# Optimization experiments

Hardware: AMD Instinct MI355X
Metric: run time of the kernel (lower is better)

## Reference

```python
import jax, jax.numpy as jnp
import numpy as np

NUM_HEADS = 4
K_RATIO = 0.01
K_NEIGHBORS = 8
DIM = 256


def setup_inputs() -> dict:
    key = jax.random.key(0)
    ks = jax.random.split(key, 11)
    d, nh = DIM, NUM_HEADS
    def lin(k, out_f, in_f):
        return jax.random.normal(k, (out_f, in_f), jnp.float32) / np.sqrt(in_f)
    return {
        "x": jax.random.normal(ks[0], (32, d, 64, 64), jnp.float32),
        # graph_modulator: Conv2d(d, d//4, 1) -> ReLU -> Conv2d(d//4, nh, 1) -> Sigmoid
        "gm_w1": lin(ks[1], d // 4, d),
        "gm_b1": jnp.zeros((d // 4,), jnp.float32),
        "gm_w2": lin(ks[2], nh, d // 4),
        "gm_b2": jnp.zeros((nh,), jnp.float32),
        # local_qkv: Linear(d, 3d, bias=False)
        "qkv_w": lin(ks[3], 3 * d, d),
        # graph_encoder: Linear(d, d//2) -> ReLU -> Linear(d//2, nh)
        "ge_w1": lin(ks[4], d // 2, d),
        "ge_b1": jnp.zeros((d // 2,), jnp.float32),
        "ge_w2": lin(ks[5], nh, d // 2),
        "ge_b2": jnp.zeros((nh,), jnp.float32),
    }


def _forward(x, gm_w1, gm_b1, gm_w2, gm_b2, qkv_w, ge_w1, ge_b1, ge_w2, ge_b2):
    B, C, H, W = x.shape
    nh = NUM_HEADS
    hd = C // nh
    scale = hd ** -0.5
    HW = H * W

    # spatial modulation: two 1x1 convs
    h1 = jax.nn.relu(jnp.einsum("bchw,oc->bohw", x, gm_w1) + gm_b1[None, :, None, None])
    spatial_mod = jax.nn.sigmoid(jnp.einsum("bchw,oc->bohw", h1, gm_w2) + gm_b2[None, :, None, None])  # [B,nh,H,W]

    # top-k pixel selection by mean-abs importance
    num_select = min(max(1, int(HW * K_RATIO)), 64)  # static
    importance = jnp.mean(jnp.abs(x), axis=1).reshape(B, HW)
    _, top_idx = jax.lax.top_k(importance, num_select)  # [B,S]

    x_flat = x.reshape(B, C, HW).transpose(0, 2, 1)  # [B,HW,C]
    sel = jnp.take_along_axis(x_flat, top_idx[:, :, None], axis=1)  # [B,S,C]

    def per_batch(feat):  # feat: [S,C]
        S = feat.shape[0]
        # kNN graph on L2-normalized features (F.normalize eps=1e-12)
        n = jnp.maximum(jnp.linalg.norm(feat, axis=1, keepdims=True), 1e-12)
        nf = feat / n
        sim = nf @ nf.T  # [S,S]
        _, nbr = jax.lax.top_k(sim, K_NEIGHBORS + 1)  # [S,k+1]
        rows = jnp.arange(S)[:, None]
        mask = jnp.zeros((S, S), feat.dtype).at[rows, nbr].set(1.0)
        mask = mask * (1.0 - jnp.eye(S, dtype=feat.dtype))  # no self-loops
        # qkv
        qkv = (feat @ qkv_w.T).reshape(S, 3, nh, hd).transpose(1, 2, 0, 3)  # [3,nh,S,hd]
        q, k, v = qkv[0], qkv[1], qkv[2]
        scores = jnp.einsum("hsd,htd->hst", q, k) * scale  # [nh,S,S]
        # graph modulation (same for every head in the torch loop)
        gw = jax.nn.relu(feat @ ge_w1.T + ge_b1) @ ge_w2.T + ge_b2  # [S,nh]
        pair = (gw @ gw.T) / nh  # mean over heads of gw_src*gw_dst
        scores = scores + 0.1 * (mask * pair)[None]
        attn = jax.nn.softmax(scores, axis=-1)
        return attn.mean(axis=(0, 2))  # [S] pixel importance

    pixel_imp = jax.vmap(per_batch)(sel)  # [B,S]

    gmw_flat = jnp.zeros((B, HW), x.dtype).at[jnp.arange(B)[:, None], top_idx].set(pixel_imp)
    graph_mod = jnp.broadcast_to(gmw_flat.reshape(B, 1, H, W), (B, nh, H, W))

    final_mod = 0.7 * spatial_mod + 0.3 * graph_mod
    return x * jnp.mean(final_mod, axis=1, keepdims=True)


def reference(x, gm_w1, gm_b1, gm_w2, gm_b2, qkv_w, ge_w1, ge_b1, ge_w2, ge_b2):
    return _forward(x, gm_w1, gm_b1, gm_w2, gm_b2, qkv_w, ge_w1, ge_b1, ge_w2, ge_b2)
```

## Files before the change

### kernel.cpp

```cpp
#include <hip/hip_runtime.h>
#include <cfloat>
#include <cstdint>

#define B_    32
#define C_    256
#define HW_   4096
#define NH_   4
#define HID_  64
#define SSEL_ 40
#define GADD_ 0.0075f

using half8_t = __attribute__((ext_vector_type(8))) _Float16;
using half4_t = __attribute__((ext_vector_type(4))) _Float16;
using f32x4_t = __attribute__((ext_vector_type(4))) float;

__global__ __launch_bounds__(256, 2) void k_mlp(
    const float* __restrict__ x,
    const float* __restrict__ w1, const float* __restrict__ b1,
    const float* __restrict__ w2, const float* __restrict__ b2,
    float* __restrict__ m, float* __restrict__ imp)
{
    __shared__ __align__(16) uint32_t WHu[64 * 128];
    __shared__ __align__(16) uint32_t XTu[256 * 32];

    const int t    = threadIdx.x;
    const int b    = blockIdx.x >> 4;
    const int p0   = (blockIdx.x & 15) << 8;
    const int lane = t & 63;
    const int wv   = t >> 6;
    const int g    = lane >> 4;
    const int lr   = lane & 15;

    #pragma unroll
    for (int i = 0; i < 16; ++i) {
        const int q   = t + (i << 8);
        const int hid = q >> 6;
        const float4 wq = *(const float4*)(w1 + ((size_t)q << 2));
        half4_t hv;
        hv[0] = (_Float16)wq.x; hv[1] = (_Float16)wq.y;
        hv[2] = (_Float16)wq.z; hv[3] = (_Float16)wq.w;
        const int col = ((q & 63) * 2) ^ ((hid & 7) << 2);
        *reinterpret_cast<half4_t*>(&WHu[hid * 128 + col]) = hv;
    }

    f32x4_t acc[4][4];
    #pragma unroll
    for (int mt = 0; mt < 4; ++mt) {
        const float4 bv = *(const float4*)(b1 + mt * 16 + g * 4);
        #pragma unroll
        for (int nt = 0; nt < 4; ++nt) {
            acc[mt][nt][0] = bv.x; acc[mt][nt][1] = bv.y;
            acc[mt][nt][2] = bv.z; acc[mt][nt][3] = bv.w;
        }
    }

    float sa = 0.f;
    const float* __restrict__ xb = x + ((size_t)b << 20) + p0 + t;

    for (int ck = 0; ck < 4; ++ck) {
        if (ck) __syncthreads();
        const float* __restrict__ xc = xb + ((size_t)(ck * 64) << 12);
        #pragma unroll
        for (int jo = 0; jo < 8; ++jo) {
            float v[8];
            #pragma unroll
            for (int e = 0; e < 8; ++e) v[e] = xc[(size_t)(jo * 8 + e) << 12];
            half8_t hv;
            #pragma unroll
            for (int e = 0; e < 8; ++e) {
                hv[e] = (_Float16)v[e];
                sa += fabsf(v[e]);
            }
            const int col = (jo * 4) ^ ((t & 7) << 2);
            *reinterpret_cast<half8_t*>(&XTu[t * 32 + col]) = hv;
        }
        __syncthreads();
        #pragma unroll
        for (int k2 = 0; k2 < 2; ++k2) {
            const int ks = ck * 2 + k2;
            half8_t af[4], bf[4];
            #pragma unroll
            for (int mt = 0; mt < 4; ++mt) {
                const int hid = mt * 16 + lr;
                const int col = (ks * 16 + g * 4) ^ ((hid & 7) << 2);
                af[mt] = *reinterpret_cast<const half8_t*>(&WHu[hid * 128 + col]);
            }
            #pragma unroll
            for (int nt = 0; nt < 4; ++nt) {
                const int px = wv * 64 + nt * 16 + lr;
                const int col = (k2 * 16 + g * 4) ^ ((px & 7) << 2);
                bf[nt] = *reinterpret_cast<const half8_t*>(&XTu[px * 32 + col]);
            }
            #pragma unroll
            for (int mt = 0; mt < 4; ++mt)
                #pragma unroll
                for (int nt = 0; nt < 4; ++nt)
                    acc[mt][nt] = __builtin_amdgcn_mfma_f32_16x16x32_f16(
                        af[mt], bf[nt], acc[mt][nt], 0, 0, 0);
        }
    }

    imp[((size_t)b << 12) + p0 + t] = sa;

    float4 w2r[4][4];
    #pragma unroll
    for (int hd = 0; hd < 4; ++hd)
        #pragma unroll
        for (int mt = 0; mt < 4; ++mt)
            w2r[hd][mt] = *(const float4*)(w2 + hd * 64 + mt * 16 + g * 4);

    #pragma unroll
    for (int nt = 0; nt < 4; ++nt) {
        float s[4] = {0.f, 0.f, 0.f, 0.f};
        #pragma unroll
        for (int mt = 0; mt < 4; ++mt) {
            const float h0 = fmaxf(acc[mt][nt][0], 0.f);
            const float h1 = fmaxf(acc[mt][nt][1], 0.f);
            const float h2 = fmaxf(acc[mt][nt][2], 0.f);
            const float h3 = fmaxf(acc[mt][nt][3], 0.f);
            #pragma unroll
            for (int hd = 0; hd < 4; ++hd) {
                s[hd] = fmaf(w2r[hd][mt].x, h0, s[hd]);
                s[hd] = fmaf(w2r[hd][mt].y, h1, s[hd]);
                s[hd] = fmaf(w2r[hd][mt].z, h2, s[hd]);
                s[hd] = fmaf(w2r[hd][mt].w, h3, s[hd]);
            }
        }
        #pragma unroll
        for (int hd = 0; hd < 4; ++hd) {
            s[hd] += __shfl_xor(s[hd], 16, 64);
            s[hd] += __shfl_xor(s[hd], 32, 64);
        }
        if (g == 0) {
            const float ssum =
                  1.f / (1.f + __expf(-(s[0] + b2[0])))
                + 1.f / (1.f + __expf(-(s[1] + b2[1])))
                + 1.f / (1.f + __expf(-(s[2] + b2[2])))
                + 1.f / (1.f + __expf(-(s[3] + b2[3])));
            m[((size_t)b << 12) + p0 + wv * 64 + nt * 16 + lr] = 0.175f * ssum;
        }
    }
}

__global__ __launch_bounds__(64) void k_topk(
    const float* __restrict__ imp, float* __restrict__ m)
{
    const int b    = blockIdx.x;
    const int lane = threadIdx.x;
    const float* __restrict__ ib = imp + (size_t)b * HW_;
    float* __restrict__ mb = m + (size_t)b * HW_;

    float v[64];
    #pragma unroll
    for (int i = 0; i < 64; ++i) v[i] = ib[i * 64 + lane];

    float g[8];
    #pragma unroll
    for (int k = 0; k < 8; ++k) {
        float gm = v[8 * k];
        #pragma unroll
        for (int i = 1; i < 8; ++i) gm = fmaxf(gm, v[8 * k + i]);
        g[k] = gm;
    }

    for (int it = 0; it < SSEL_; ++it) {
        float lm = g[0];
        #pragma unroll
        for (int k = 1; k < 8; ++k) lm = fmaxf(lm, g[k]);
        float wm = lm;
        #pragma unroll
        for (int off = 32; off >= 1; off >>= 1)
            wm = fmaxf(wm, __shfl_xor(wm, off, 64));
        #pragma unroll
        for (int k = 0; k < 8; ++k) {
            if (__any(g[k] == wm)) {
                int gi = -1;
                #pragma unroll
                for (int i = 0; i < 8; ++i) {
                    if (v[8 * k + i] == wm) {
                        gi = (8 * k + i) * 64 + lane;
                        v[8 * k + i] = -FLT_MAX;
                    }
                }
                float gm = v[8 * k];
                #pragma unroll
                for (int i = 1; i < 8; ++i) gm = fmaxf(gm, v[8 * k + i]);
                g[k] = gm;
                if (gi >= 0) mb[gi] += GADD_;
            }
        }
    }
}

__global__ __launch_bounds__(256) void k_apply(
    const float4* __restrict__ x4, const float* __restrict__ m,
    float4* __restrict__ o4)
{
    const size_t i = (size_t)blockIdx.x * 256 + threadIdx.x;
    const size_t flat = i << 2;
    const int b = (int)(flat >> 20);
    const int p = (int)(flat & (HW_ - 1));
    const float4 mv = *(const float4*)(m + ((size_t)b << 12) + p);
    const float4 xv = x4[i];
    float4 r;
    r.x = xv.x * mv.x; r.y = xv.y * mv.y;
    r.z = xv.z * mv.z; r.w = xv.w * mv.w;
    o4[i] = r;
}

extern "C" void kernel_launch(void* const* d_in, const int* in_sizes, int n_in,
                              void* d_out, int out_size, void* d_ws, size_t ws_size,
                              hipStream_t stream)
{
    const float* x  = (const float*)d_in[0];
    const float* w1 = (const float*)d_in[1];
    const float* b1 = (const float*)d_in[2];
    const float* w2 = (const float*)d_in[3];
    const float* b2 = (const float*)d_in[4];

    float* m   = (float*)d_ws;
    float* imp = m + (size_t)B_ * HW_;
    float* out = (float*)d_out;

    k_mlp<<<dim3(B_ * (HW_ / 256)), dim3(256), 0, stream>>>(x, w1, b1, w2, b2, m, imp);
    k_topk<<<dim3(B_), dim3(64), 0, stream>>>(imp, m);
    const int n4 = (B_ * C_ * HW_) / 4;
    k_apply<<<dim3(n4 / 256), dim3(256), 0, stream>>>((const float4*)x, m, (float4*)out);
}
```

Baseline: 293.6 us.

## Load x directly into MFMA B fragments and halve pixels per block

The x tile is no longer staged through shared memory. Each lane loads its 8-channel slice straight from global memory into the half8 B operand, and the partial abs-sums are reduced across lane groups with shuffles. The block covers 128 pixels instead of 256, which doubles the grid, and launch bounds rise to 4 blocks per CU to raise occupancy now that LDS is only the weight tile. This removes the LDS round trip and the per-chunk barriers. The cost is that global loads become 16-pixel segments of 64 bytes instead of full 256-pixel rows, and the per-block fp16 conversion of w1 is repeated twice as often.

```diff
diff --git a/kernel.cpp b/kernel.cpp
--- a/kernel.cpp
+++ b/kernel.cpp
@@ -14,18 +14,17 @@
 using half4_t = __attribute__((ext_vector_type(4))) _Float16;
 using f32x4_t = __attribute__((ext_vector_type(4))) float;
 
-__global__ __launch_bounds__(256, 2) void k_mlp(
+__global__ __launch_bounds__(256, 4) void k_mlp(
     const float* __restrict__ x,
     const float* __restrict__ w1, const float* __restrict__ b1,
     const float* __restrict__ w2, const float* __restrict__ b2,
     float* __restrict__ m, float* __restrict__ imp)
 {
     __shared__ __align__(16) uint32_t WHu[64 * 128];
-    __shared__ __align__(16) uint32_t XTu[256 * 32];
 
     const int t    = threadIdx.x;
-    const int b    = blockIdx.x >> 4;
-    const int p0   = (blockIdx.x & 15) << 8;
+    const int b    = blockIdx.x >> 5;
+    const int p0   = (blockIdx.x & 31) << 7;
     const int lane = t & 63;
     const int wv   = t >> 6;
     const int g    = lane >> 4;
@@ -43,42 +42,41 @@
         *reinterpret_cast<half4_t*>(&WHu[hid * 128 + col]) = hv;
     }
 
-    f32x4_t acc[4][4];
+    f32x4_t acc[4][2];
     #pragma unroll
     for (int mt = 0; mt < 4; ++mt) {
         const float4 bv = *(const float4*)(b1 + mt * 16 + g * 4);
         #pragma unroll
-        for (int nt = 0; nt < 4; ++nt) {
+        for (int nt = 0; nt < 2; ++nt) {
             acc[mt][nt][0] = bv.x; acc[mt][nt][1] = bv.y;
             acc[mt][nt][2] = bv.z; acc[mt][nt][3] = bv.w;
         }
     }
-
-    float sa = 0.f;
-    const float* __restrict__ xb = x + ((size_t)b << 20) + p0 + t;
+    __syncthreads();
+
+    float sa[2] = {0.f, 0.f};
+    const float* __restrict__ xp =
+        x + ((size_t)b << 20) + (size_t)(g * 8) * HW_ + p0 + wv * 32 + lr;
 
     for (int ck = 0; ck < 4; ++ck) {
-        if (ck) __syncthreads();
-        const float* __restrict__ xc = xb + ((size_t)(ck * 64) << 12);
-        #pragma unroll
-        for (int jo = 0; jo < 8; ++jo) {
-            float v[8];
-            #pragma unroll
-            for (int e = 0; e < 8; ++e) v[e] = xc[(size_t)(jo * 8 + e) << 12];
-            half8_t hv;
-            #pragma unroll
-            for (int e = 0; e < 8; ++e) {
-                hv[e] = (_Float16)v[e];
-                sa += fabsf(v[e]);
-            }
-            const int col = (jo * 4) ^ ((t & 7) << 2);
-            *reinterpret_cast<half8_t*>(&XTu[t * 32 + col]) = hv;
-        }
-        __syncthreads();
         #pragma unroll
         for (int k2 = 0; k2 < 2; ++k2) {
             const int ks = ck * 2 + k2;
-            half8_t af[4], bf[4];
+            half8_t bf[2];
+            #pragma unroll
+            for (int nt = 0; nt < 2; ++nt) {
+                const float* __restrict__ xc =
+                    xp + (size_t)(ck * 64 + k2 * 32) * HW_ + nt * 16;
+                float v[8];
+                #pragma unroll
+                for (int e = 0; e < 8; ++e) v[e] = xc[(size_t)e * HW_];
+                #pragma unroll
+                for (int e = 0; e < 8; ++e) {
+                    bf[nt][e] = (_Float16)v[e];
+                    sa[nt] += fabsf(v[e]);
+                }
+            }
+            half8_t af[4];
             #pragma unroll
             for (int mt = 0; mt < 4; ++mt) {
                 const int hid = mt * 16 + lr;
@@ -86,21 +84,22 @@
                 af[mt] = *reinterpret_cast<const half8_t*>(&WHu[hid * 128 + col]);
             }
             #pragma unroll
-            for (int nt = 0; nt < 4; ++nt) {
-                const int px = wv * 64 + nt * 16 + lr;
-                const int col = (k2 * 16 + g * 4) ^ ((px & 7) << 2);
-                bf[nt] = *reinterpret_cast<const half8_t*>(&XTu[px * 32 + col]);
-            }
-            #pragma unroll
             for (int mt = 0; mt < 4; ++mt)
                 #pragma unroll
-                for (int nt = 0; nt < 4; ++nt)
+                for (int nt = 0; nt < 2; ++nt)
                     acc[mt][nt] = __builtin_amdgcn_mfma_f32_16x16x32_f16(
                         af[mt], bf[nt], acc[mt][nt], 0, 0, 0);
         }
     }
 
-    imp[((size_t)b << 12) + p0 + t] = sa;
+    #pragma unroll
+    for (int nt = 0; nt < 2; ++nt) {
+        float s = sa[nt];
+        s += __shfl_xor(s, 16, 64);
+        s += __shfl_xor(s, 32, 64);
+        if (g == 0)
+            imp[((size_t)b << 12) + p0 + wv * 32 + nt * 16 + lr] = s;
+    }
 
     float4 w2r[4][4];
     #pragma unroll
@@ -110,7 +109,7 @@
             w2r[hd][mt] = *(const float4*)(w2 + hd * 64 + mt * 16 + g * 4);
 
     #pragma unroll
-    for (int nt = 0; nt < 4; ++nt) {
+    for (int nt = 0; nt < 2; ++nt) {
         float s[4] = {0.f, 0.f, 0.f, 0.f};
         #pragma unroll
         for (int mt = 0; mt < 4; ++mt) {
@@ -137,7 +136,7 @@
                 + 1.f / (1.f + __expf(-(s[1] + b2[1])))
                 + 1.f / (1.f + __expf(-(s[2] + b2[2])))
                 + 1.f / (1.f + __expf(-(s[3] + b2[3])));
-            m[((size_t)b << 12) + p0 + wv * 64 + nt * 16 + lr] = 0.175f * ssum;
+            m[((size_t)b << 12) + p0 + wv * 32 + nt * 16 + lr] = 0.175f * ssum;
         }
     }
 }
@@ -222,7 +221,7 @@
     float* imp = m + (size_t)B_ * HW_;
     float* out = (float*)d_out;
 
-    k_mlp<<<dim3(B_ * (HW_ / 256)), dim3(256), 0, stream>>>(x, w1, b1, w2, b2, m, imp);
+    k_mlp<<<dim3(B_ * (HW_ / 128)), dim3(256), 0, stream>>>(x, w1, b1, w2, b2, m, imp);
     k_topk<<<dim3(B_), dim3(64), 0, stream>>>(imp, m);
     const int n4 = (B_ * C_ * HW_) / 4;
     k_apply<<<dim3(n4 / 256), dim3(256), 0, stream>>>((const float4*)x, m, (float4*)out);
```

New measurement: 307.9 us. 4.9% more time.
